# Performance work log

Hardware: AMD Instinct MI355X
Metric: run time of the kernel (lower is better)

## Reference

```python
import jax, jax.numpy as jnp
import numpy as np

B, IN_F, OUT_F, K = 8192, 1024, 4096, 2
S = 64  # sqrt(OUT_F)


def setup_inputs() -> dict:
    key = jax.random.key(0)
    k1, k2, k3, k4 = jax.random.split(key, 4)
    x = jax.random.normal(k1, (B, IN_F), dtype=jnp.float32)
    y = jax.random.normal(k2, (B, OUT_F), dtype=jnp.float32)
    weight = jax.random.normal(k3, (OUT_F, IN_F), dtype=jnp.float32) * (1.0 / np.sqrt(IN_F))
    bias = jax.random.normal(k4, (OUT_F,), dtype=jnp.float32) * (1.0 / np.sqrt(IN_F))
    return {"x": x, "y": y, "weight": weight, "bias": bias}


def reference(x, y, weight, bias):
    # fused GEMM + bias + residual add epilogue
    out_lin = jnp.einsum('bk,nk->bn', x, weight) + bias + y  # (B, OUT_F)
    feat = out_lin.reshape(B, S, S)
    # AvgPool2d(kernel=K, stride=K)
    s_out = S // K
    pooled = feat.reshape(B, s_out, K, s_out, K).mean(axis=(2, 4))  # (B, s_out, s_out)
    # divide by global mean of the pooled map
    mean_val = pooled.mean()
    normed = pooled / mean_val
    return normed[:, None, :, :]  # (B, 1, s_out, s_out)
```

## Files before the change

### kernel.cpp

```cpp
#include <hip/hip_runtime.h>
#include <stdint.h>


#define KDIM 1024
#define NP   1024
#define BM 256
#define BN 128
#define BK 64
#define NBLK 256

typedef __bf16 bf16x8 __attribute__((ext_vector_type(8)));
typedef float f32x4 __attribute__((ext_vector_type(4)));
typedef _Float16 f16x4 __attribute__((ext_vector_type(4)));

__device__ __forceinline__ unsigned f2bf(float f) {
  union { float f; unsigned u; } v; v.f = f;
  unsigned r = v.u + 0x7fffu + ((v.u >> 16) & 1u);
  return r >> 16;
}

__device__ __forceinline__ void gload_lds16(const void* g, void* l) {
  __builtin_amdgcn_global_load_lds(
      (const __attribute__((address_space(1))) void*)g,
      (__attribute__((address_space(3))) void*)l, 16, 0, 0);
}

__global__ void k_prep(const float* __restrict__ x, const float* __restrict__ W,
                       const float* __restrict__ bias,
                       unsigned short* __restrict__ xb, unsigned short* __restrict__ wp,
                       float* __restrict__ biasp) {
  int b = blockIdx.x;
  int t = threadIdx.x;
  if (b < 4096) {
    int i = b * 256 + t;
    const float4* x4 = (const float4*)x;
    float4 a = x4[i * 2], c = x4[i * 2 + 1];
    uint4 o;
    o.x = f2bf(a.x) | (f2bf(a.y) << 16);
    o.y = f2bf(a.z) | (f2bf(a.w) << 16);
    o.z = f2bf(c.x) | (f2bf(c.y) << 16);
    o.w = f2bf(c.z) | (f2bf(c.w) << 16);
    ((uint4*)xb)[i] = o;
  } else {
    int o = b - 4096;
    int r0 = ((o >> 5) << 7) + ((o & 31) << 1);
    const float4* W4 = (const float4*)W;
    float4 w0 = W4[(r0) * 256 + t];
    float4 w1 = W4[(r0 + 1) * 256 + t];
    float4 w2 = W4[(r0 + 64) * 256 + t];
    float4 w3 = W4[(r0 + 65) * 256 + t];
    float ax = 0.25f * (w0.x + w1.x + w2.x + w3.x);
    float ay = 0.25f * (w0.y + w1.y + w2.y + w3.y);
    float az = 0.25f * (w0.z + w1.z + w2.z + w3.z);
    float aw = 0.25f * (w0.w + w1.w + w2.w + w3.w);
    uint2 pk;
    pk.x = f2bf(ax) | (f2bf(ay) << 16);
    pk.y = f2bf(az) | (f2bf(aw) << 16);
    ((uint2*)wp)[o * 256 + t] = pk;
    if (t == 0)
      biasp[o] = 0.25f * (bias[r0] + bias[r0 + 1] + bias[r0 + 64] + bias[r0 + 65]);
  }
}

__global__ __launch_bounds__(1024, 4) void k_gemm(
    const unsigned short* __restrict__ xb, const unsigned short* __restrict__ wp,
    const float* __restrict__ biasp, const float* __restrict__ y,
    float* __restrict__ out, _Float16* __restrict__ ph,
    float* __restrict__ partials, int use16) {
  __shared__ char smem[98304];

  int bid = blockIdx.x;
  int wg = (bid & 7) * 32 + (bid >> 3);
  int bm0 = (wg >> 3) * BM;
  int bn0 = (wg & 7) * BN;

  int tid = threadIdx.x;
  int lane = tid & 63;
  int wid = tid >> 6;
  int wr = wid >> 1, wc = wid & 1;

  f32x4 acc[2][4];
#pragma unroll
  for (int i = 0; i < 2; i++)
#pragma unroll
    for (int j = 0; j < 4; j++) acc[i][j] = (f32x4)0.0f;

  int srow = tid >> 3;
  int scol = (((lane & 7) ^ (lane >> 3)) << 3);
  const unsigned short* aSrc = xb + (size_t)(bm0 + srow) * KDIM + scol;
  const unsigned short* bSrc = wp + (size_t)(bn0 + srow) * KDIM + scol;
  int ldsOff = wid * 1024;

  int rbase = (lane & 15) * 128;
  int xorv = (lane & 7) << 4;
  int cb0 = (((lane >> 4) * 16)) ^ xorv;
  int cb1 = ((64 + (lane >> 4) * 16)) ^ xorv;

  const float2* y2 = (const float2*)y;
  int r_l = (lane >> 4) * 4;
  int c_l = lane & 15;
  int yrb = bm0 + wr * 32 + r_l;
  int yb[4];
#pragma unroll
  for (int ni = 0; ni < 4; ++ni) {
    int col = bn0 + wc * 64 + ni * 16 + c_l;
    yb[ni] = ((col >> 5) << 6) + (col & 31);
  }
  float2 yin[2][4];

#define STAGE_P1(buf, ks)                                                      \
  {                                                                            \
    int k0 = (ks) * BK;                                                        \
    char* ab = smem + (buf) * 49152 + ldsOff;                                  \
    gload_lds16(aSrc + k0, ab);                                                \
    gload_lds16(aSrc + (size_t)128 * KDIM + k0, ab + 16384);                   \
  }
#define STAGE_P2(buf, ks)                                                      \
  {                                                                            \
    int k0 = (ks) * BK;                                                        \
    char* bb = smem + (buf) * 49152 + 32768 + ldsOff;                          \
    gload_lds16(bSrc + k0, bb);                                                \
  }

#define YLD(slot, s, q)                                                        \
  {                                                                            \
    const float2* pp = y2 +                                                    \
        (size_t)(yrb + (((q) >> 4) * 16) + ((q) & 3)) * 2048 + yb[((q) >> 2) & 3]; \
    asm volatile("global_load_dwordx2 %0, %1, off"                             \
                 : "=v"(yin[slot][s]) : "v"(pp) : "memory");                   \
    asm volatile("global_load_dwordx2 %0, %1, off offset:256"                  \
                 : "=v"(yin[slot][(s) + 1]) : "v"(pp) : "memory");             \
  }
#define YLOAD(slot, t) { YLD(slot, 0, 2 * (t)) YLD(slot, 2, 2 * (t) + 1) }
#define YCONS(slot, p)                                                         \
  {                                                                            \
    acc[(2 * (p)) >> 4][((2 * (p)) >> 2) & 3][(2 * (p)) & 3] +=                \
        0.25f * ((yin[slot][0].x + yin[slot][0].y) +                           \
                 (yin[slot][1].x + yin[slot][1].y));                           \
    acc[(2 * (p) + 1) >> 4][((2 * (p) + 1) >> 2) & 3][(2 * (p) + 1) & 3] +=    \
        0.25f * ((yin[slot][2].x + yin[slot][2].y) +                           \
                 (yin[slot][3].x + yin[slot][3].y));                           \
  }

#define FRAGS(av, bv, cbv, Ab, Bb)                                             \
  {                                                                            \
    _Pragma("unroll")                                                          \
    for (int mi = 0; mi < 2; ++mi)                                             \
      av[mi] = *(const bf16x8*)((Ab) + (wr * 32 + mi * 16) * 128 + rbase + (cbv)); \
    _Pragma("unroll")                                                          \
    for (int ni = 0; ni < 4; ++ni)                                             \
      bv[ni] = *(const bf16x8*)((Bb) + (wc * 64 + ni * 16) * 128 + rbase + (cbv)); \
  }
#define MM8(av, bv)                                                            \
  {                                                                            \
    _Pragma("unroll")                                                          \
    for (int mi = 0; mi < 2; ++mi)                                             \
      _Pragma("unroll")                                                        \
      for (int ni = 0; ni < 4; ++ni)                                           \
        acc[mi][ni] = __builtin_amdgcn_mfma_f32_16x16x32_bf16(                 \
            av[mi], bv[ni], acc[mi][ni], 0, 0, 0);                             \
  }

#define TILE(t, WSTR)                                                          \
  {                                                                            \
    asm volatile(WSTR ::: "memory");                                           \
    __builtin_amdgcn_sched_barrier(0);                                         \
    __builtin_amdgcn_s_barrier();                                              \
    if ((t) >= 2) YCONS(((t) - 2) & 1, (t) - 2);                               \
    const char* Ab = smem + ((t) & 1) * 49152;                                 \
    const char* Bb = Ab + 32768;                                               \
    bf16x8 a0[2], b0[4];                                                       \
    FRAGS(a0, b0, cb0, Ab, Bb);                                                \
    if ((t) < 15) STAGE_P1(((t) + 1) & 1, (t) + 1);                            \
    asm volatile("s_waitcnt lgkmcnt(0)" ::: "memory");                         \
    __builtin_amdgcn_sched_barrier(0);                                         \
    __builtin_amdgcn_s_setprio(1);                                             \
    MM8(a0, b0);                                                               \
    __builtin_amdgcn_s_setprio(0);                                             \
    bf16x8 a1[2], b1[4];                                                       \
    FRAGS(a1, b1, cb1, Ab, Bb);                                                \
    if ((t) < 15) STAGE_P2(((t) + 1) & 1, (t) + 1);                            \
    YLOAD((t) & 1, t);                                                         \
    asm volatile("s_waitcnt lgkmcnt(0)" ::: "memory");                         \
    __builtin_amdgcn_sched_barrier(0);                                         \
    __builtin_amdgcn_s_setprio(1);                                             \
    MM8(a1, b1);                                                               \
    __builtin_amdgcn_s_setprio(0);                                             \
  }

  STAGE_P1(0, 0);
  STAGE_P2(0, 0);

  TILE(0,  "s_waitcnt vmcnt(0)")
  TILE(1,  "s_waitcnt vmcnt(4)")
  TILE(2,  "s_waitcnt vmcnt(4)")
  TILE(3,  "s_waitcnt vmcnt(4)")
  TILE(4,  "s_waitcnt vmcnt(4)")
  TILE(5,  "s_waitcnt vmcnt(4)")
  TILE(6,  "s_waitcnt vmcnt(4)")
  TILE(7,  "s_waitcnt vmcnt(4)")
  TILE(8,  "s_waitcnt vmcnt(4)")
  TILE(9,  "s_waitcnt vmcnt(4)")
  TILE(10, "s_waitcnt vmcnt(4)")
  TILE(11, "s_waitcnt vmcnt(4)")
  TILE(12, "s_waitcnt vmcnt(4)")
  TILE(13, "s_waitcnt vmcnt(4)")
  TILE(14, "s_waitcnt vmcnt(4)")
  TILE(15, "s_waitcnt vmcnt(4)")

  asm volatile("s_waitcnt vmcnt(0)" ::: "memory");
  __builtin_amdgcn_sched_barrier(0);
  YCONS(0, 14);
  YCONS(1, 15);

  float tsum = 0.f;
  float bpv[4];
#pragma unroll
  for (int ni = 0; ni < 4; ++ni) bpv[ni] = biasp[bn0 + wc * 64 + ni * 16 + c_l];
#pragma unroll
  for (int mi = 0; mi < 2; ++mi) {
#pragma unroll
    for (int ni = 0; ni < 4; ++ni) {
      int col = bn0 + wc * 64 + ni * 16 + c_l;
#pragma unroll
      for (int j = 0; j < 4; ++j) {
        int row = bm0 + wr * 32 + mi * 16 + r_l + j;
        float val = acc[mi][ni][j] + bpv[ni];
        size_t o = (size_t)row * NP + col;
        if (use16) ph[o] = (_Float16)val;
        else out[o] = val;
        tsum += val;
      }
    }
  }
#pragma unroll
  for (int off = 32; off > 0; off >>= 1) tsum += __shfl_down(tsum, off);
  float* sm = (float*)smem;
  __syncthreads();
  if (lane == 0) sm[wid] = tsum;
  __syncthreads();
  if (tid == 0) {
    float s0 = ((sm[0] + sm[1]) + (sm[2] + sm[3])) +
               ((sm[4] + sm[5]) + (sm[6] + sm[7]));
    float s1 = ((sm[8] + sm[9]) + (sm[10] + sm[11])) +
               ((sm[12] + sm[13]) + (sm[14] + sm[15]));
    partials[bid] = s0 + s1;
  }
}

__global__ void k_norm(float* __restrict__ out, const _Float16* __restrict__ ph,
                       const float* __restrict__ partials, int use16) {
  __shared__ float s[256];
  int t = threadIdx.x;
  s[t] = partials[t];
  __syncthreads();
#pragma unroll
  for (int off = 128; off > 0; off >>= 1) {
    if (t < off) s[t] += s[t + off];
    __syncthreads();
  }
  float inv = 8388608.0f / s[0];
  int i = blockIdx.x * 256 + t;
  float4* o4 = (float4*)out;
  if (use16) {
    f16x4 hv = ((const f16x4*)ph)[i];
    float4 v;
    v.x = (float)hv[0] * inv;
    v.y = (float)hv[1] * inv;
    v.z = (float)hv[2] * inv;
    v.w = (float)hv[3] * inv;
    o4[i] = v;
  } else {
    float4 v = o4[i];
    v.x *= inv; v.y *= inv; v.z *= inv; v.w *= inv;
    o4[i] = v;
  }
}

extern "C" void kernel_launch(void* const* d_in, const int* in_sizes, int n_in,
                              void* d_out, int out_size, void* d_ws, size_t ws_size,
                              hipStream_t stream) {
  (void)in_sizes; (void)n_in; (void)out_size;
  const float* x = (const float*)d_in[0];
  const float* y = (const float*)d_in[1];
  const float* W = (const float*)d_in[2];
  const float* bias = (const float*)d_in[3];
  float* out = (float*)d_out;

  char* ws = (char*)d_ws;
  unsigned short* xb = (unsigned short*)(ws);
  unsigned short* wp = (unsigned short*)(ws + 16777216);
  float* biasp = (float*)(ws + 16777216 + 2097152);
  float* partials = (float*)(ws + 16777216 + 2097152 + 4096);
  _Float16* ph = (_Float16*)(ws + 20971520);
  int use16 = (ws_size >= (size_t)20971520 + 16777216) ? 1 : 0;

  hipLaunchKernelGGL(k_prep, dim3(5120), dim3(256), 0, stream, x, W, bias, xb, wp, biasp);
  hipLaunchKernelGGL(k_gemm, dim3(NBLK), dim3(1024), 0, stream, xb, wp, biasp, y, out, ph, partials, use16);
  hipLaunchKernelGGL(k_norm, dim3(8192), dim3(256), 0, stream, out, ph, partials, use16);
}
```

Before: 58.15 us.

## Shrink GEMM tiles to 128x128x32 with 512 blocks of 512 threads

Halves the GEMM block tile in M and the K step, doubling the grid to 512 workgroups of 8 waves with a 32-step K loop and a smaller 32KB double-buffered LDS. This fills more CUs on the 256-CU part and allows more blocks per CU, at the cost of less data reuse per tile and more barriers per K step. The LDS swizzle, y-prefetch pipeline and partial-sum reduction are reworked to match, and the norm kernel now combines 512 partials.

Result: slower. 59.54 us (+2.4%).

```diff
diff --git a/kernel.cpp b/kernel.cpp
--- a/kernel.cpp
+++ b/kernel.cpp
@@ -4,10 +4,11 @@
 
 #define KDIM 1024
 #define NP   1024
-#define BM 256
+#define BM 128
 #define BN 128
-#define BK 64
-#define NBLK 256
+#define BK 32
+#define NT 32
+#define NBLK 512
 
 typedef __bf16 bf16x8 __attribute__((ext_vector_type(8)));
 typedef float f32x4 __attribute__((ext_vector_type(4)));
@@ -62,15 +63,15 @@
   }
 }
 
-__global__ __launch_bounds__(1024, 4) void k_gemm(
+__global__ __launch_bounds__(512, 4) void k_gemm(
     const unsigned short* __restrict__ xb, const unsigned short* __restrict__ wp,
     const float* __restrict__ biasp, const float* __restrict__ y,
     float* __restrict__ out, _Float16* __restrict__ ph,
     float* __restrict__ partials, int use16) {
-  __shared__ char smem[98304];
+  __shared__ char smem[32768];
 
   int bid = blockIdx.x;
-  int wg = (bid & 7) * 32 + (bid >> 3);
+  int wg = (bid & 7) * 64 + (bid >> 3);
   int bm0 = (wg >> 3) * BM;
   int bn0 = (wg & 7) * BN;
 
@@ -85,16 +86,14 @@
 #pragma unroll
     for (int j = 0; j < 4; j++) acc[i][j] = (f32x4)0.0f;
 
-  int srow = tid >> 3;
-  int scol = (((lane & 7) ^ (lane >> 3)) << 3);
+  int srow = tid >> 2;
+  int scol = (((tid & 3) ^ ((tid >> 3) & 3)) << 3);
   const unsigned short* aSrc = xb + (size_t)(bm0 + srow) * KDIM + scol;
   const unsigned short* bSrc = wp + (size_t)(bn0 + srow) * KDIM + scol;
   int ldsOff = wid * 1024;
 
-  int rbase = (lane & 15) * 128;
-  int xorv = (lane & 7) << 4;
-  int cb0 = (((lane >> 4) * 16)) ^ xorv;
-  int cb1 = ((64 + (lane >> 4) * 16)) ^ xorv;
+  int rbase = (lane & 15) * 64;
+  int rchunk = (((lane >> 4) ^ ((lane >> 1) & 3)) << 4);
 
   const float2* y2 = (const float2*)y;
   int r_l = (lane >> 4) * 4;
@@ -106,112 +105,100 @@
     int col = bn0 + wc * 64 + ni * 16 + c_l;
     yb[ni] = ((col >> 5) << 6) + (col & 31);
   }
-  float2 yin[2][4];
-
-#define STAGE_P1(buf, ks)                                                      \
+  float2 yin[2][2];
+
+#define STAGE(buf, ks)                                                         \
   {                                                                            \
     int k0 = (ks) * BK;                                                        \
-    char* ab = smem + (buf) * 49152 + ldsOff;                                  \
+    char* ab = smem + (buf) * 16384 + ldsOff;                                  \
+    char* bb = smem + (buf) * 16384 + 8192 + ldsOff;                           \
     gload_lds16(aSrc + k0, ab);                                                \
-    gload_lds16(aSrc + (size_t)128 * KDIM + k0, ab + 16384);                   \
-  }
-#define STAGE_P2(buf, ks)                                                      \
-  {                                                                            \
-    int k0 = (ks) * BK;                                                        \
-    char* bb = smem + (buf) * 49152 + 32768 + ldsOff;                          \
     gload_lds16(bSrc + k0, bb);                                                \
   }
 
-#define YLD(slot, s, q)                                                        \
+#define YLOAD(slot, q)                                                         \
   {                                                                            \
     const float2* pp = y2 +                                                    \
         (size_t)(yrb + (((q) >> 4) * 16) + ((q) & 3)) * 2048 + yb[((q) >> 2) & 3]; \
     asm volatile("global_load_dwordx2 %0, %1, off"                             \
-                 : "=v"(yin[slot][s]) : "v"(pp) : "memory");                   \
+                 : "=v"(yin[slot][0]) : "v"(pp) : "memory");                   \
     asm volatile("global_load_dwordx2 %0, %1, off offset:256"                  \
-                 : "=v"(yin[slot][(s) + 1]) : "v"(pp) : "memory");             \
-  }
-#define YLOAD(slot, t) { YLD(slot, 0, 2 * (t)) YLD(slot, 2, 2 * (t) + 1) }
-#define YCONS(slot, p)                                                         \
-  {                                                                            \
-    acc[(2 * (p)) >> 4][((2 * (p)) >> 2) & 3][(2 * (p)) & 3] +=                \
+                 : "=v"(yin[slot][1]) : "v"(pp) : "memory");                   \
+  }
+#define YCONS(slot, q)                                                         \
+  {                                                                            \
+    acc[(q) >> 4][((q) >> 2) & 3][(q) & 3] +=                                  \
         0.25f * ((yin[slot][0].x + yin[slot][0].y) +                           \
                  (yin[slot][1].x + yin[slot][1].y));                           \
-    acc[(2 * (p) + 1) >> 4][((2 * (p) + 1) >> 2) & 3][(2 * (p) + 1) & 3] +=    \
-        0.25f * ((yin[slot][2].x + yin[slot][2].y) +                           \
-                 (yin[slot][3].x + yin[slot][3].y));                           \
-  }
-
-#define FRAGS(av, bv, cbv, Ab, Bb)                                             \
-  {                                                                            \
+  }
+
+#define TILE(t, WSTR)                                                          \
+  {                                                                            \
+    asm volatile(WSTR ::: "memory");                                           \
+    __builtin_amdgcn_sched_barrier(0);                                         \
+    __builtin_amdgcn_s_barrier();                                              \
+    if ((t) >= 2) YCONS(((t) - 2) & 1, (t) - 2);                               \
+    const char* Ab = smem + ((t) & 1) * 16384;                                 \
+    const char* Bb = Ab + 8192;                                                \
+    bf16x8 a0[2], b0[4];                                                       \
     _Pragma("unroll")                                                          \
     for (int mi = 0; mi < 2; ++mi)                                             \
-      av[mi] = *(const bf16x8*)((Ab) + (wr * 32 + mi * 16) * 128 + rbase + (cbv)); \
+      a0[mi] = *(const bf16x8*)(Ab + (wr * 32 + mi * 16) * 64 + rbase + rchunk); \
     _Pragma("unroll")                                                          \
     for (int ni = 0; ni < 4; ++ni)                                             \
-      bv[ni] = *(const bf16x8*)((Bb) + (wc * 64 + ni * 16) * 128 + rbase + (cbv)); \
-  }
-#define MM8(av, bv)                                                            \
-  {                                                                            \
+      b0[ni] = *(const bf16x8*)(Bb + (wc * 64 + ni * 16) * 64 + rbase + rchunk); \
+    if ((t) < NT - 1) STAGE(((t) + 1) & 1, (t) + 1);                           \
+    YLOAD((t) & 1, t);                                                         \
+    asm volatile("s_waitcnt lgkmcnt(0)" ::: "memory");                         \
+    __builtin_amdgcn_sched_barrier(0);                                         \
+    __builtin_amdgcn_s_setprio(1);                                             \
     _Pragma("unroll")                                                          \
     for (int mi = 0; mi < 2; ++mi)                                             \
       _Pragma("unroll")                                                        \
       for (int ni = 0; ni < 4; ++ni)                                           \
         acc[mi][ni] = __builtin_amdgcn_mfma_f32_16x16x32_bf16(                 \
-            av[mi], bv[ni], acc[mi][ni], 0, 0, 0);                             \
-  }
-
-#define TILE(t, WSTR)                                                          \
-  {                                                                            \
-    asm volatile(WSTR ::: "memory");                                           \
-    __builtin_amdgcn_sched_barrier(0);                                         \
-    __builtin_amdgcn_s_barrier();                                              \
-    if ((t) >= 2) YCONS(((t) - 2) & 1, (t) - 2);                               \
-    const char* Ab = smem + ((t) & 1) * 49152;                                 \
-    const char* Bb = Ab + 32768;                                               \
-    bf16x8 a0[2], b0[4];                                                       \
-    FRAGS(a0, b0, cb0, Ab, Bb);                                                \
-    if ((t) < 15) STAGE_P1(((t) + 1) & 1, (t) + 1);                            \
-    asm volatile("s_waitcnt lgkmcnt(0)" ::: "memory");                         \
-    __builtin_amdgcn_sched_barrier(0);                                         \
-    __builtin_amdgcn_s_setprio(1);                                             \
-    MM8(a0, b0);                                                               \
+            a0[mi], b0[ni], acc[mi][ni], 0, 0, 0);                             \
     __builtin_amdgcn_s_setprio(0);                                             \
-    bf16x8 a1[2], b1[4];                                                       \
-    FRAGS(a1, b1, cb1, Ab, Bb);                                                \
-    if ((t) < 15) STAGE_P2(((t) + 1) & 1, (t) + 1);                            \
-    YLOAD((t) & 1, t);                                                         \
-    asm volatile("s_waitcnt lgkmcnt(0)" ::: "memory");                         \
-    __builtin_amdgcn_sched_barrier(0);                                         \
-    __builtin_amdgcn_s_setprio(1);                                             \
-    MM8(a1, b1);                                                               \
-    __builtin_amdgcn_s_setprio(0);                                             \
-  }
-
-  STAGE_P1(0, 0);
-  STAGE_P2(0, 0);
-
+  }
+
+  STAGE(0, 0);
   TILE(0,  "s_waitcnt vmcnt(0)")
-  TILE(1,  "s_waitcnt vmcnt(4)")
-  TILE(2,  "s_waitcnt vmcnt(4)")
-  TILE(3,  "s_waitcnt vmcnt(4)")
-  TILE(4,  "s_waitcnt vmcnt(4)")
-  TILE(5,  "s_waitcnt vmcnt(4)")
-  TILE(6,  "s_waitcnt vmcnt(4)")
-  TILE(7,  "s_waitcnt vmcnt(4)")
-  TILE(8,  "s_waitcnt vmcnt(4)")
-  TILE(9,  "s_waitcnt vmcnt(4)")
-  TILE(10, "s_waitcnt vmcnt(4)")
-  TILE(11, "s_waitcnt vmcnt(4)")
-  TILE(12, "s_waitcnt vmcnt(4)")
-  TILE(13, "s_waitcnt vmcnt(4)")
-  TILE(14, "s_waitcnt vmcnt(4)")
-  TILE(15, "s_waitcnt vmcnt(4)")
+  TILE(1,  "s_waitcnt vmcnt(2)")
+  TILE(2,  "s_waitcnt vmcnt(2)")
+  TILE(3,  "s_waitcnt vmcnt(2)")
+  TILE(4,  "s_waitcnt vmcnt(2)")
+  TILE(5,  "s_waitcnt vmcnt(2)")
+  TILE(6,  "s_waitcnt vmcnt(2)")
+  TILE(7,  "s_waitcnt vmcnt(2)")
+  TILE(8,  "s_waitcnt vmcnt(2)")
+  TILE(9,  "s_waitcnt vmcnt(2)")
+  TILE(10, "s_waitcnt vmcnt(2)")
+  TILE(11, "s_waitcnt vmcnt(2)")
+  TILE(12, "s_waitcnt vmcnt(2)")
+  TILE(13, "s_waitcnt vmcnt(2)")
+  TILE(14, "s_waitcnt vmcnt(2)")
+  TILE(15, "s_waitcnt vmcnt(2)")
+  TILE(16, "s_waitcnt vmcnt(2)")
+  TILE(17, "s_waitcnt vmcnt(2)")
+  TILE(18, "s_waitcnt vmcnt(2)")
+  TILE(19, "s_waitcnt vmcnt(2)")
+  TILE(20, "s_waitcnt vmcnt(2)")
+  TILE(21, "s_waitcnt vmcnt(2)")
+  TILE(22, "s_waitcnt vmcnt(2)")
+  TILE(23, "s_waitcnt vmcnt(2)")
+  TILE(24, "s_waitcnt vmcnt(2)")
+  TILE(25, "s_waitcnt vmcnt(2)")
+  TILE(26, "s_waitcnt vmcnt(2)")
+  TILE(27, "s_waitcnt vmcnt(2)")
+  TILE(28, "s_waitcnt vmcnt(2)")
+  TILE(29, "s_waitcnt vmcnt(2)")
+  TILE(30, "s_waitcnt vmcnt(2)")
+  TILE(31, "s_waitcnt vmcnt(2)")
 
   asm volatile("s_waitcnt vmcnt(0)" ::: "memory");
   __builtin_amdgcn_sched_barrier(0);
-  YCONS(0, 14);
-  YCONS(1, 15);
+  YCONS(0, 30);
+  YCONS(1, 31);
 
   float tsum = 0.f;
   float bpv[4];
@@ -239,20 +226,16 @@
   __syncthreads();
   if (lane == 0) sm[wid] = tsum;
   __syncthreads();
-  if (tid == 0) {
-    float s0 = ((sm[0] + sm[1]) + (sm[2] + sm[3])) +
-               ((sm[4] + sm[5]) + (sm[6] + sm[7]));
-    float s1 = ((sm[8] + sm[9]) + (sm[10] + sm[11])) +
-               ((sm[12] + sm[13]) + (sm[14] + sm[15]));
-    partials[bid] = s0 + s1;
-  }
+  if (tid == 0)
+    partials[bid] = ((sm[0] + sm[1]) + (sm[2] + sm[3])) +
+                    ((sm[4] + sm[5]) + (sm[6] + sm[7]));
 }
 
 __global__ void k_norm(float* __restrict__ out, const _Float16* __restrict__ ph,
                        const float* __restrict__ partials, int use16) {
   __shared__ float s[256];
   int t = threadIdx.x;
-  s[t] = partials[t];
+  s[t] = partials[t] + partials[t + 256];
   __syncthreads();
 #pragma unroll
   for (int off = 128; off > 0; off >>= 1) {
@@ -296,6 +279,6 @@
   int use16 = (ws_size >= (size_t)20971520 + 16777216) ? 1 : 0;
 
   hipLaunchKernelGGL(k_prep, dim3(5120), dim3(256), 0, stream, x, W, bias, xb, wp, biasp);
-  hipLaunchKernelGGL(k_gemm, dim3(NBLK), dim3(1024), 0, stream, xb, wp, biasp, y, out, ph, partials, use16);
+  hipLaunchKernelGGL(k_gemm, dim3(NBLK), dim3(512), 0, stream, xb, wp, biasp, y, out, ph, partials, use16);
   hipLaunchKernelGGL(k_norm, dim3(8192), dim3(256), 0, stream, out, ph, partials, use16);
 }
```
